# Kernel tuning notes

Measured on AMD Instinct MI355X. Metric: run time of the kernel, lower is better.

The kernel has to match this reference:

```python
import jax, jax.numpy as jnp
import numpy as np

H, W = 4096, 4096
KH, KW = 15, 15


def setup_inputs() -> dict:
    key = jax.random.key(0)
    k1, k2 = jax.random.split(key)
    x = jax.random.normal(k1, (H, W), dtype=jnp.float32)
    weight = jax.random.normal(k2, (KH, KW), dtype=jnp.float32)
    bias = jnp.zeros((1,), dtype=jnp.float32)
    return {"x": x, "weight": weight, "bias": bias}


def reference(x, weight, bias):
    # corr2d: valid cross-correlation of 2D x with 2D kernel, output [H-KH+1, W-KW+1]
    # lax conv with NCHW/OIHW layout computes cross-correlation (no kernel flip),
    # identical to the torch per-pixel slice-multiply-sum loop.
    out = jax.lax.conv_general_dilated(
        x[None, None, :, :],            # [1,1,H,W]
        weight[None, None, :, :],       # [1,1,KH,KW]
        window_strides=(1, 1),
        padding="VALID",
    )[0, 0]                             # [H-KH+1, W-KW+1]
    return out + bias  # bias is shape [1], broadcasts like torch
```

## Files before the change

kernel.cpp:

```cpp
#include <hip/hip_runtime.h>


#define HIN 4096
#define WIN 4096
#define KH 15
#define KW 15
#define OH (HIN - KH + 1)
#define OW (WIN - KW + 1)

#define BX 64
#define BY 64
#define XROWS (BY + KH - 1)
#define XCOLS 80
#define LDSW 88
#define BTAB (XROWS * LDSW)
#define NSH (BTAB + 15 * 64 * 8)

typedef short bf16x8 __attribute__((ext_vector_type(8)));
typedef float f32x4  __attribute__((ext_vector_type(4)));

static __device__ inline short f2bf(float f) {
    unsigned u = __float_as_uint(f);
    u += 0x7fffu + ((u >> 16) & 1u);
    return (short)(u >> 16);
}

__global__ __launch_bounds__(256)
void conv2d_mfma(const float* __restrict__ x,
                 const float* __restrict__ w,
                 const float* __restrict__ bias,
                 float* __restrict__ out) {
    __shared__ short lds[NSH];

    const int tid = threadIdx.x;
    const int ox0 = blockIdx.x * BX;
    const int oy0 = blockIdx.y * BY;

    for (int f = tid; f < XROWS * (XCOLS / 4); f += 256) {
        const int r  = f / (XCOLS / 4);
        const int c4 = (f - r * (XCOLS / 4)) * 4;
        int gy = oy0 + r;
        if (gy > HIN - 1) gy = HIN - 1;
        const int gx = ox0 + c4;
        float4 v;
        if (gx + 3 <= WIN - 1) {
            v = *reinterpret_cast<const float4*>(&x[(size_t)gy * WIN + gx]);
        } else {
            const float* row = &x[(size_t)gy * WIN];
            const int x0 = (gx + 0 > WIN - 1) ? WIN - 1 : gx + 0;
            const int x1 = (gx + 1 > WIN - 1) ? WIN - 1 : gx + 1;
            const int x2 = (gx + 2 > WIN - 1) ? WIN - 1 : gx + 2;
            const int x3 = (gx + 3 > WIN - 1) ? WIN - 1 : gx + 3;
            v = make_float4(row[x0], row[x1], row[x2], row[x3]);
        }
        short4 s;
        s.x = f2bf(v.x); s.y = f2bf(v.y); s.z = f2bf(v.z); s.w = f2bf(v.w);
        *reinterpret_cast<short4*>(&lds[r * LDSW + c4]) = s;
    }

    for (int e = tid; e < 15 * 64; e += 256) {
        const int kh = e >> 6;
        const int L  = e & 63;
        const int n  = L & 15;
        const int q  = L >> 4;
        bf16x8 bv;
#pragma unroll
        for (int j = 0; j < 8; ++j) {
            const int d = q * 8 + j - n;
            bv[j] = (d >= 0 && d < KW) ? f2bf(w[kh * KW + d]) : (short)0;
        }
        *reinterpret_cast<bf16x8*>(&lds[BTAB + e * 8]) = bv;
    }
    __syncthreads();

    const int lane = tid & 63;
    const int wv   = tid >> 6;
    const int m    = lane & 15;
    const int q    = lane >> 4;

    bf16x8 B[KH];
#pragma unroll
    for (int kh = 0; kh < KH; ++kh)
        B[kh] = *reinterpret_cast<const bf16x8*>(&lds[BTAB + (kh * 64 + lane) * 8]);

    f32x4 acc[4];
#pragma unroll
    for (int t = 0; t < 4; ++t) acc[t] = (f32x4){0.f, 0.f, 0.f, 0.f};

    const short* abase = &lds[(wv * 16 + m) * LDSW + q * 8];
#pragma unroll
    for (int kh = 0; kh < KH; ++kh) {
#pragma unroll
        for (int t = 0; t < 4; ++t) {
            const bf16x8 a =
                *reinterpret_cast<const bf16x8*>(abase + kh * LDSW + t * 16);
            acc[t] = __builtin_amdgcn_mfma_f32_16x16x32_bf16(a, B[kh], acc[t], 0, 0, 0);
        }
    }

    const float b0 = bias[0];
    const int row0 = oy0 + wv * 16 + q * 4;
#pragma unroll
    for (int t = 0; t < 4; ++t) {
        const int col = ox0 + t * 16 + m;
        if (col < OW) {
#pragma unroll
            for (int r = 0; r < 4; ++r) {
                const int row = row0 + r;
                if (row < OH)
                    out[(size_t)row * OW + col] = acc[t][r] + b0;
            }
        }
    }
}

extern "C" void kernel_launch(void* const* d_in, const int* in_sizes, int n_in,
                              void* d_out, int out_size, void* d_ws, size_t ws_size,
                              hipStream_t stream) {
    const float* x    = (const float*)d_in[0];
    const float* w    = (const float*)d_in[1];
    const float* bias = (const float*)d_in[2];
    float* out        = (float*)d_out;

    dim3 grid((OW + BX - 1) / BX, (OH + BY - 1) / BY);
    dim3 block(256);
    conv2d_mfma<<<grid, block, 0, stream>>>(x, w, bias, out);
}
```

Baseline: 155.5 us.

## March each block down four row tiles with double-buffered LDS prefetch

Each block now processes four consecutive 64-row output tiles rather than one. While the current tile is computed, the next input tile is prefetched from global memory into registers and then written to a second LDS buffer. The weight table is built once per block and amortized across the four tiles. Grid size shrinks fourfold, and the change adds register pressure from the seven float4 prefetch slots and the unroll.

```diff
diff --git a/kernel.cpp b/kernel.cpp
--- a/kernel.cpp
+++ b/kernel.cpp
@@ -9,12 +9,14 @@
 #define OW (WIN - KW + 1)
 
 #define BX 64
-#define BY 64
-#define XROWS (BY + KH - 1)
+#define BYSTEP 64
+#define SSTEPS 4
+#define XROWS (BYSTEP + KH - 1)
 #define XCOLS 80
 #define LDSW 88
-#define BTAB (XROWS * LDSW)
-#define NSH (BTAB + 15 * 64 * 8)
+#define BUFSH (XROWS * LDSW)
+#define NSLOT (XROWS * (XCOLS / 4))
+#define NPF 7
 
 typedef short bf16x8 __attribute__((ext_vector_type(8)));
 typedef float f32x4  __attribute__((ext_vector_type(4)));
@@ -25,92 +27,130 @@
     return (short)(u >> 16);
 }
 
-__global__ __launch_bounds__(256)
-void conv2d_mfma(const float* __restrict__ x,
-                 const float* __restrict__ w,
-                 const float* __restrict__ bias,
-                 float* __restrict__ out) {
-    __shared__ short lds[NSH];
+static __device__ inline float4 load_clamped(const float* __restrict__ x,
+                                             int gy, int gx) {
+    if (gy > HIN - 1) gy = HIN - 1;
+    if (gx + 3 <= WIN - 1) {
+        return *reinterpret_cast<const float4*>(&x[(size_t)gy * WIN + gx]);
+    }
+    const float* row = &x[(size_t)gy * WIN];
+    const int x0 = (gx + 0 > WIN - 1) ? WIN - 1 : gx + 0;
+    const int x1 = (gx + 1 > WIN - 1) ? WIN - 1 : gx + 1;
+    const int x2 = (gx + 2 > WIN - 1) ? WIN - 1 : gx + 2;
+    const int x3 = (gx + 3 > WIN - 1) ? WIN - 1 : gx + 3;
+    return make_float4(row[x0], row[x1], row[x2], row[x3]);
+}
 
-    const int tid = threadIdx.x;
-    const int ox0 = blockIdx.x * BX;
-    const int oy0 = blockIdx.y * BY;
+__global__ __launch_bounds__(256, 4)
+void conv2d_mfma_march(const float* __restrict__ x,
+                       const float* __restrict__ w,
+                       const float* __restrict__ bias,
+                       float* __restrict__ out) {
+    __shared__ short lds[2 * BUFSH];
 
-    for (int f = tid; f < XROWS * (XCOLS / 4); f += 256) {
-        const int r  = f / (XCOLS / 4);
-        const int c4 = (f - r * (XCOLS / 4)) * 4;
-        int gy = oy0 + r;
-        if (gy > HIN - 1) gy = HIN - 1;
-        const int gx = ox0 + c4;
-        float4 v;
-        if (gx + 3 <= WIN - 1) {
-            v = *reinterpret_cast<const float4*>(&x[(size_t)gy * WIN + gx]);
-        } else {
-            const float* row = &x[(size_t)gy * WIN];
-            const int x0 = (gx + 0 > WIN - 1) ? WIN - 1 : gx + 0;
-            const int x1 = (gx + 1 > WIN - 1) ? WIN - 1 : gx + 1;
-            const int x2 = (gx + 2 > WIN - 1) ? WIN - 1 : gx + 2;
-            const int x3 = (gx + 3 > WIN - 1) ? WIN - 1 : gx + 3;
-            v = make_float4(row[x0], row[x1], row[x2], row[x3]);
-        }
-        short4 s;
-        s.x = f2bf(v.x); s.y = f2bf(v.y); s.z = f2bf(v.z); s.w = f2bf(v.w);
-        *reinterpret_cast<short4*>(&lds[r * LDSW + c4]) = s;
-    }
+    const int tid  = threadIdx.x;
+    const int lane = tid & 63;
+    const int wv   = tid >> 6;
+    const int m    = lane & 15;
+    const int q    = lane >> 4;
+    const int ox0  = blockIdx.x * BX;
+    const int ybase = blockIdx.y * (SSTEPS * BYSTEP);
 
     for (int e = tid; e < 15 * 64; e += 256) {
         const int kh = e >> 6;
         const int L  = e & 63;
         const int n  = L & 15;
-        const int q  = L >> 4;
+        const int qq = L >> 4;
         bf16x8 bv;
 #pragma unroll
         for (int j = 0; j < 8; ++j) {
-            const int d = q * 8 + j - n;
+            const int d = qq * 8 + j - n;
             bv[j] = (d >= 0 && d < KW) ? f2bf(w[kh * KW + d]) : (short)0;
         }
-        *reinterpret_cast<bf16x8*>(&lds[BTAB + e * 8]) = bv;
+        *reinterpret_cast<bf16x8*>(&lds[e * 8]) = bv;
+    }
+    __syncthreads();
+    bf16x8 B[KH];
+#pragma unroll
+    for (int kh = 0; kh < KH; ++kh)
+        B[kh] = *reinterpret_cast<const bf16x8*>(&lds[(kh * 64 + lane) * 8]);
+    __syncthreads();
+
+    for (int f = tid; f < NSLOT; f += 256) {
+        const int r  = f / (XCOLS / 4);
+        const int c4 = (f - r * (XCOLS / 4)) * 4;
+        const float4 v = load_clamped(x, ybase + r, ox0 + c4);
+        short4 s;
+        s.x = f2bf(v.x); s.y = f2bf(v.y); s.z = f2bf(v.z); s.w = f2bf(v.w);
+        *reinterpret_cast<short4*>(&lds[r * LDSW + c4]) = s;
     }
     __syncthreads();
 
-    const int lane = tid & 63;
-    const int wv   = tid >> 6;
-    const int m    = lane & 15;
-    const int q    = lane >> 4;
+    const float b0 = bias[0];
 
-    bf16x8 B[KH];
+    for (int s = 0; s < SSTEPS; ++s) {
+        const short* cur = &lds[(s & 1) * BUFSH];
+        short*       nxt = &lds[((s + 1) & 1) * BUFSH];
+        const int    oy0 = ybase + s * BYSTEP;
+        const bool   has_next = (s + 1 < SSTEPS);
+
+        float4 pf[NPF];
+        if (has_next) {
 #pragma unroll
-    for (int kh = 0; kh < KH; ++kh)
-        B[kh] = *reinterpret_cast<const bf16x8*>(&lds[BTAB + (kh * 64 + lane) * 8]);
+            for (int i = 0; i < NPF; ++i) {
+                const int f = tid + i * 256;
+                if (f < NSLOT) {
+                    const int r  = f / (XCOLS / 4);
+                    const int c4 = (f - r * (XCOLS / 4)) * 4;
+                    pf[i] = load_clamped(x, oy0 + BYSTEP + r, ox0 + c4);
+                }
+            }
+        }
 
-    f32x4 acc[4];
+        f32x4 acc[4];
 #pragma unroll
-    for (int t = 0; t < 4; ++t) acc[t] = (f32x4){0.f, 0.f, 0.f, 0.f};
+        for (int t = 0; t < 4; ++t) acc[t] = (f32x4){0.f, 0.f, 0.f, 0.f};
 
-    const short* abase = &lds[(wv * 16 + m) * LDSW + q * 8];
+        const short* abase = cur + (wv * 16 + m) * LDSW + q * 8;
 #pragma unroll
-    for (int kh = 0; kh < KH; ++kh) {
+        for (int kh = 0; kh < KH; ++kh) {
+#pragma unroll
+            for (int t = 0; t < 4; ++t) {
+                const bf16x8 a =
+                    *reinterpret_cast<const bf16x8*>(abase + kh * LDSW + t * 16);
+                acc[t] = __builtin_amdgcn_mfma_f32_16x16x32_bf16(a, B[kh], acc[t], 0, 0, 0);
+            }
+        }
+
+        const int row0 = oy0 + wv * 16 + q * 4;
 #pragma unroll
         for (int t = 0; t < 4; ++t) {
-            const bf16x8 a =
-                *reinterpret_cast<const bf16x8*>(abase + kh * LDSW + t * 16);
-            acc[t] = __builtin_amdgcn_mfma_f32_16x16x32_bf16(a, B[kh], acc[t], 0, 0, 0);
-        }
-    }
-
-    const float b0 = bias[0];
-    const int row0 = oy0 + wv * 16 + q * 4;
+            const int col = ox0 + t * 16 + m;
+            if (col < OW) {
 #pragma unroll
-    for (int t = 0; t < 4; ++t) {
-        const int col = ox0 + t * 16 + m;
-        if (col < OW) {
-#pragma unroll
-            for (int r = 0; r < 4; ++r) {
-                const int row = row0 + r;
-                if (row < OH)
-                    out[(size_t)row * OW + col] = acc[t][r] + b0;
+                for (int r = 0; r < 4; ++r) {
+                    const int row = row0 + r;
+                    if (row < OH)
+                        out[(size_t)row * OW + col] = acc[t][r] + b0;
+                }
             }
         }
+
+        if (has_next) {
+#pragma unroll
+            for (int i = 0; i < NPF; ++i) {
+                const int f = tid + i * 256;
+                if (f < NSLOT) {
+                    const int r  = f / (XCOLS / 4);
+                    const int c4 = (f - r * (XCOLS / 4)) * 4;
+                    short4 sv;
+                    sv.x = f2bf(pf[i].x); sv.y = f2bf(pf[i].y);
+                    sv.z = f2bf(pf[i].z); sv.w = f2bf(pf[i].w);
+                    *reinterpret_cast<short4*>(&nxt[r * LDSW + c4]) = sv;
+                }
+            }
+        }
+        __syncthreads();
     }
 }
 
@@ -122,7 +162,7 @@
     const float* bias = (const float*)d_in[2];
     float* out        = (float*)d_out;
 
-    dim3 grid((OW + BX - 1) / BX, (OH + BY - 1) / BY);
+    dim3 grid((OW + BX - 1) / BX, (OH + SSTEPS * BYSTEP - 1) / (SSTEPS * BYSTEP));
     dim3 block(256);
-    conv2d_mfma<<<grid, block, 0, stream>>>(x, w, bias, out);
+    conv2d_mfma_march<<<grid, block, 0, stream>>>(x, w, bias, out);
 }
```

New measurement: 185.8 us. +19.5%, slower.

## Enlarge conv tile to 128x128 and build banded weights in registers

Applied to the files above, without the earlier changes.

Doubles the output tile in both dimensions, so each wave computes a 32x128 strip with 16 MFMA accumulators instead of 16x64. This cuts the halo overhead per output and reduces the block count. The banded Toeplitz weight table is no longer staged through LDS; each lane builds its 15 bf16x8 B fragments straight from global weights. The cost is higher register pressure, larger LDS use per block and fewer blocks to spread across CUs, which may lower occupancy and latency hiding.

```diff
diff --git a/kernel.cpp b/kernel.cpp
--- a/kernel.cpp
+++ b/kernel.cpp
@@ -8,13 +8,12 @@
 #define OH (HIN - KH + 1)
 #define OW (WIN - KW + 1)
 
-#define BX 64
-#define BY 64
+#define BX 128
+#define BY 128
 #define XROWS (BY + KH - 1)
-#define XCOLS 80
-#define LDSW 88
-#define BTAB (XROWS * LDSW)
-#define NSH (BTAB + 15 * 64 * 8)
+#define XCOLS 144
+#define LDSW 152
+#define NSLOT (XROWS * (XCOLS / 4))
 
 typedef short bf16x8 __attribute__((ext_vector_type(8)));
 typedef float f32x4  __attribute__((ext_vector_type(4)));
@@ -26,89 +25,92 @@
 }
 
 __global__ __launch_bounds__(256)
-void conv2d_mfma(const float* __restrict__ x,
-                 const float* __restrict__ w,
-                 const float* __restrict__ bias,
-                 float* __restrict__ out) {
-    __shared__ short lds[NSH];
+void conv2d_mfma_big(const float* __restrict__ x,
+                     const float* __restrict__ w,
+                     const float* __restrict__ bias,
+                     float* __restrict__ out) {
+    __shared__ short lds[XROWS * LDSW];
 
-    const int tid = threadIdx.x;
-    const int ox0 = blockIdx.x * BX;
-    const int oy0 = blockIdx.y * BY;
-
-    for (int f = tid; f < XROWS * (XCOLS / 4); f += 256) {
-        const int r  = f / (XCOLS / 4);
-        const int c4 = (f - r * (XCOLS / 4)) * 4;
-        int gy = oy0 + r;
-        if (gy > HIN - 1) gy = HIN - 1;
-        const int gx = ox0 + c4;
-        float4 v;
-        if (gx + 3 <= WIN - 1) {
-            v = *reinterpret_cast<const float4*>(&x[(size_t)gy * WIN + gx]);
-        } else {
-            const float* row = &x[(size_t)gy * WIN];
-            const int x0 = (gx + 0 > WIN - 1) ? WIN - 1 : gx + 0;
-            const int x1 = (gx + 1 > WIN - 1) ? WIN - 1 : gx + 1;
-            const int x2 = (gx + 2 > WIN - 1) ? WIN - 1 : gx + 2;
-            const int x3 = (gx + 3 > WIN - 1) ? WIN - 1 : gx + 3;
-            v = make_float4(row[x0], row[x1], row[x2], row[x3]);
-        }
-        short4 s;
-        s.x = f2bf(v.x); s.y = f2bf(v.y); s.z = f2bf(v.z); s.w = f2bf(v.w);
-        *reinterpret_cast<short4*>(&lds[r * LDSW + c4]) = s;
-    }
-
-    for (int e = tid; e < 15 * 64; e += 256) {
-        const int kh = e >> 6;
-        const int L  = e & 63;
-        const int n  = L & 15;
-        const int q  = L >> 4;
-        bf16x8 bv;
-#pragma unroll
-        for (int j = 0; j < 8; ++j) {
-            const int d = q * 8 + j - n;
-            bv[j] = (d >= 0 && d < KW) ? f2bf(w[kh * KW + d]) : (short)0;
-        }
-        *reinterpret_cast<bf16x8*>(&lds[BTAB + e * 8]) = bv;
-    }
-    __syncthreads();
-
+    const int tid  = threadIdx.x;
     const int lane = tid & 63;
     const int wv   = tid >> 6;
     const int m    = lane & 15;
     const int q    = lane >> 4;
+    const int ox0  = blockIdx.x * BX;
+    const int oy0  = blockIdx.y * BY;
+
+    for (int i = 0; i < (NSLOT + 255) / 256; ++i) {
+        const int f = tid + i * 256;
+        if (f < NSLOT) {
+            const int r  = f / (XCOLS / 4);
+            const int c4 = (f - r * (XCOLS / 4)) * 4;
+            int gy = oy0 + r;
+            if (gy > HIN - 1) gy = HIN - 1;
+            const int gx = ox0 + c4;
+            float4 v;
+            if (gx + 3 <= WIN - 1) {
+                v = *reinterpret_cast<const float4*>(&x[(size_t)gy * WIN + gx]);
+            } else {
+                const float* row = &x[(size_t)gy * WIN];
+                const int x0 = (gx + 0 > WIN - 1) ? WIN - 1 : gx + 0;
+                const int x1 = (gx + 1 > WIN - 1) ? WIN - 1 : gx + 1;
+                const int x2 = (gx + 2 > WIN - 1) ? WIN - 1 : gx + 2;
+                const int x3 = (gx + 3 > WIN - 1) ? WIN - 1 : gx + 3;
+                v = make_float4(row[x0], row[x1], row[x2], row[x3]);
+            }
+            short4 s;
+            s.x = f2bf(v.x); s.y = f2bf(v.y); s.z = f2bf(v.z); s.w = f2bf(v.w);
+            *reinterpret_cast<short4*>(&lds[r * LDSW + c4]) = s;
+        }
+    }
 
     bf16x8 B[KH];
 #pragma unroll
-    for (int kh = 0; kh < KH; ++kh)
-        B[kh] = *reinterpret_cast<const bf16x8*>(&lds[BTAB + (kh * 64 + lane) * 8]);
+    for (int kh = 0; kh < KH; ++kh) {
+#pragma unroll
+        for (int j = 0; j < 8; ++j) {
+            const int d = q * 8 + j - m;
+            B[kh][j] = (d >= 0 && d < KW) ? f2bf(w[kh * KW + d]) : (short)0;
+        }
+    }
 
-    f32x4 acc[4];
+    __syncthreads();
+
+    f32x4 acc[2][8];
 #pragma unroll
-    for (int t = 0; t < 4; ++t) acc[t] = (f32x4){0.f, 0.f, 0.f, 0.f};
+    for (int rv = 0; rv < 2; ++rv)
+#pragma unroll
+        for (int t = 0; t < 8; ++t) acc[rv][t] = (f32x4){0.f, 0.f, 0.f, 0.f};
 
-    const short* abase = &lds[(wv * 16 + m) * LDSW + q * 8];
+    const short* abase = &lds[(wv * 32 + m) * LDSW + q * 8];
 #pragma unroll
     for (int kh = 0; kh < KH; ++kh) {
 #pragma unroll
-        for (int t = 0; t < 4; ++t) {
-            const bf16x8 a =
-                *reinterpret_cast<const bf16x8*>(abase + kh * LDSW + t * 16);
-            acc[t] = __builtin_amdgcn_mfma_f32_16x16x32_bf16(a, B[kh], acc[t], 0, 0, 0);
+        for (int rv = 0; rv < 2; ++rv) {
+#pragma unroll
+            for (int t = 0; t < 8; ++t) {
+                const bf16x8 a = *reinterpret_cast<const bf16x8*>(
+                    abase + (kh + rv * 16) * LDSW + t * 16);
+                acc[rv][t] =
+                    __builtin_amdgcn_mfma_f32_16x16x32_bf16(a, B[kh], acc[rv][t], 0, 0, 0);
+            }
         }
     }
 
     const float b0 = bias[0];
-    const int row0 = oy0 + wv * 16 + q * 4;
 #pragma unroll
-    for (int t = 0; t < 4; ++t) {
-        const int col = ox0 + t * 16 + m;
-        if (col < OW) {
+    for (int rv = 0; rv < 2; ++rv) {
+        const int row0 = oy0 + wv * 32 + rv * 16 + q * 4;
 #pragma unroll
-            for (int r = 0; r < 4; ++r) {
-                const int row = row0 + r;
-                if (row < OH)
-                    out[(size_t)row * OW + col] = acc[t][r] + b0;
+        for (int t = 0; t < 8; ++t) {
+            const int col = ox0 + t * 16 + m;
+            if (col < OW) {
+#pragma unroll
+                for (int r = 0; r < 4; ++r) {
+                    const int row = row0 + r;
+                    if (row < OH)
+                        out[(size_t)row * OW + col] = acc[rv][t][r] + b0;
+                }
             }
         }
     }
@@ -124,5 +126,5 @@
 
     dim3 grid((OW + BX - 1) / BX, (OH + BY - 1) / BY);
     dim3 block(256);
-    conv2d_mfma<<<grid, block, 0, stream>>>(x, w, bias, out);
+    conv2d_mfma_big<<<grid, block, 0, stream>>>(x, w, bias, out);
 }
```

Result: slower. 161.1 us (+3.6%).
